# Performance work log

Hardware: AMD Instinct MI355X
Metric: run time of the kernel (lower is better)

The kernel has to match this reference:

```python
import jax, jax.numpy as jnp
import numpy as np

N, E, D, L = 10000, 160000, 512, 3
NEG_SLOPE = 0.2
LN_EPS = 1e-5


def setup_inputs() -> dict:
    key = jax.random.key(0)
    ks = jax.random.split(key, 16)
    def rn(k, shape, scale=0.02):
        return jax.random.normal(k, shape, dtype=jnp.float32) * scale
    return {
        "x": jax.random.normal(ks[0], (N, D), dtype=jnp.float32),
        "edge_attr": jax.random.normal(ks[1], (E, 2), dtype=jnp.float32),
        "emb_inv_W": rn(ks[2], (D, D)), "emb_inv_b": jnp.zeros((D,), jnp.float32),
        "emb_org_W": rn(ks[3], (D, D)), "emb_org_b": jnp.zeros((D,), jnp.float32),
        "gat_Wl": rn(ks[4], (L, D, D)), "gat_bl": jnp.zeros((L, D), jnp.float32),
        "gat_Wr": rn(ks[5], (L, D, D)), "gat_br": jnp.zeros((L, D), jnp.float32),
        "gat_We": rn(ks[6], (L, 2, D)),
        "gat_att": rn(ks[7], (L, D), 0.1),
        "gat_bias": jnp.zeros((L, D), jnp.float32),
        "ln_g": jnp.ones((L, D), jnp.float32), "ln_b": jnp.zeros((L, D), jnp.float32),
        "lin0_W": rn(ks[8], (2 * D, D)), "lin0_b": jnp.zeros((D,), jnp.float32),
        "lin1_W": rn(ks[9], (2 * D, D)), "lin1_b": jnp.zeros((D,), jnp.float32),
        "edge_index": jax.random.randint(ks[10], (2, E), 0, N, dtype=jnp.int32),
        "n_inv": 4000,
        "n_unknown": 3000,
    }


def _layernorm(x, g, b):
    m = jnp.mean(x, axis=-1, keepdims=True)
    v = jnp.mean((x - m) ** 2, axis=-1, keepdims=True)
    return (x - m) * jax.lax.rsqrt(v + LN_EPS) * g + b


def _gatv2(x, src, dst, edge_attr, Wl, bl, Wr, br, We, att, bias):
    # single-head GATv2: e_ij = att . leaky_relu(Wl x_j + Wr x_i + We e_ij)
    xl = x @ Wl + bl                                  # [N,D] source transform
    xr = x @ Wr + br                                  # [N,D] target transform
    m = xl[src] + xr[dst] + edge_attr @ We            # [E,D]
    s = jax.nn.leaky_relu(m, NEG_SLOPE) @ att         # [E] attention logits
    smax = jax.ops.segment_max(s, dst, num_segments=N)  # per-target max
    a = jnp.exp(s - smax[dst])
    denom = jax.ops.segment_sum(a, dst, num_segments=N)
    alpha = a / jnp.where(denom[dst] > 0, denom[dst], 1.0)  # [E]
    out = jax.ops.segment_sum(alpha[:, None] * xl[src], dst, num_segments=N)
    return out + bias


def _forward(x, edge_attr, emb_inv_W, emb_inv_b, emb_org_W, emb_org_b,
             gat_Wl, gat_bl, gat_Wr, gat_br, gat_We, gat_att, gat_bias,
             ln_g, ln_b, lin0_W, lin0_b, lin1_W, lin1_b,
             edge_index, n_inv, n_unknown):
    src, dst = edge_index[0], edge_index[1]
    x0 = x[:n_inv] @ emb_inv_W + emb_inv_b           # [n_inv, D]
    x1 = x[n_inv:] @ emb_org_W + emb_org_b           # [N-n_inv, D]
    h = jnp.concatenate([x0, x1], axis=0)            # [N, D]
    for k in range(L):
        hc = _gatv2(h, src, dst, edge_attr,
                    gat_Wl[k], gat_bl[k], gat_Wr[k], gat_br[k],
                    gat_We[k], gat_att[k], gat_bias[k])
        h = jax.nn.relu(_layernorm(hc + h, ln_g[k], ln_b[k]))
    y0 = jnp.concatenate([x0, h[:n_inv]], axis=-1) @ lin0_W + lin0_b          # [n_inv, D]
    y1 = jnp.concatenate([x1[-n_unknown:], h[-n_unknown:]], axis=-1) @ lin1_W + lin1_b  # [n_unknown, D]
    return y0 @ y1.T                                  # [n_inv, n_unknown]


def reference(x, edge_attr, emb_inv_W, emb_inv_b, emb_org_W, emb_org_b,
              gat_Wl, gat_bl, gat_Wr, gat_br, gat_We, gat_att, gat_bias,
              ln_g, ln_b, lin0_W, lin0_b, lin1_W, lin1_b,
              edge_index, n_inv, n_unknown):
    return _forward(x, edge_attr, emb_inv_W, emb_inv_b, emb_org_W, emb_org_b,
                    gat_Wl, gat_bl, gat_Wr, gat_br, gat_We, gat_att, gat_bias,
                    ln_g, ln_b, lin0_W, lin0_b, lin1_W, lin1_b,
                    edge_index, n_inv, n_unknown)
```

## Files before the change

kernel.cpp:

```cpp
#include <hip/hip_runtime.h>
#include <cstddef>
#include <cstdint>

namespace {

using u16 = unsigned short;
typedef __attribute__((ext_vector_type(8))) unsigned short u16x8;
typedef __attribute__((ext_vector_type(8))) short bf16x8;
typedef __attribute__((ext_vector_type(4))) float f32x4;

constexpr int kN    = 10000;
constexpr int kE    = 160000;
constexpr int kD    = 512;
constexpr int kNinv = 4000;
constexpr int kNunk = 3000;
constexpr int kND   = kN * kD;
constexpr float kNegSlope = 0.2f;
constexpr float kLnEps    = 1e-5f;

__device__ __forceinline__ float bf2f(u16 u) {
  return __uint_as_float((unsigned)u << 16);
}
__device__ __forceinline__ u16 f2bf(float f) {
  unsigned u = __float_as_uint(f);
  return (u16)((u + 0x7FFFu + ((u >> 16) & 1u)) >> 16);
}

__device__ __forceinline__ void gload_lds16(const void* g, void* l) {
  __builtin_amdgcn_global_load_lds(
      (const __attribute__((address_space(1))) void*)(unsigned long long)(uintptr_t)g,
      (__attribute__((address_space(3))) void*)(unsigned)(uintptr_t)l,
      16, 0, 0);
}

template <bool WRITE_F32, bool WRITE_BF16>
__global__ __launch_bounds__(256) void gemm_bf16(
    const u16* __restrict__ A1, const u16* __restrict__ A2,
    const u16* __restrict__ BT, const float* __restrict__ bias,
    float* __restrict__ Cf, u16* __restrict__ Cb, u16* __restrict__ Cb2,
    int nsplit, int M, int N, int K, int ldc) {
  __shared__ u16 As[128 * 64];
  __shared__ u16 Bs[128 * 64];
  const int tid  = threadIdx.x;
  const int lane = tid & 63;
  const int wid  = tid >> 6;
  const int bm = blockIdx.x * 128;
  const int bn = blockIdx.y * 128;
  const int wr = (wid >> 1) * 64;
  const int wc = (wid & 1) * 64;

  f32x4 acc[4][4];
#pragma unroll
  for (int m = 0; m < 4; ++m)
#pragma unroll
    for (int n = 0; n < 4; ++n) acc[m][n] = (f32x4){0.f, 0.f, 0.f, 0.f};

  const int srow = lane >> 3;
  const int slot = lane & 7;
  const size_t astride = (A2 != nullptr) ? 512 : (size_t)K;

  for (int k0 = 0; k0 < K; k0 += 64) {
    const u16* Ap = A1;
    int kof = k0;
    if (A2 != nullptr && k0 >= 512) { Ap = A2; kof = k0 - 512; }
#pragma unroll
    for (int t = 0; t < 4; ++t) {
      const int inst = wid * 4 + t;
      const int row  = inst * 8 + srow;
      const int scol = ((slot ^ (row & 7)) << 4);
      const int ar   = min(bm + row, M - 1);
      gload_lds16((const char*)Ap + ((size_t)ar * astride + kof) * 2 + scol,
                  (char*)As + inst * 1024);
    }
#pragma unroll
    for (int t = 0; t < 4; ++t) {
      const int inst = wid * 4 + t;
      const int row  = inst * 8 + srow;
      const int scol = ((slot ^ (row & 7)) << 4);
      const int bc   = min(bn + row, N - 1);
      gload_lds16((const char*)BT + ((size_t)bc * K + k0) * 2 + scol,
                  (char*)Bs + inst * 1024);
    }
    asm volatile("s_waitcnt vmcnt(0)" ::: "memory");
    __syncthreads();

#pragma unroll
    for (int kk = 0; kk < 2; ++kk) {
      bf16x8 af[4], bfr[4];
#pragma unroll
      for (int m = 0; m < 4; ++m) {
        const int r = wr + m * 16 + (lane & 15);
        const int s = kk * 4 + (lane >> 4);
        af[m] = *(const bf16x8*)((const char*)As + r * 128 + ((s ^ (r & 7)) << 4));
      }
#pragma unroll
      for (int n = 0; n < 4; ++n) {
        const int c = wc + n * 16 + (lane & 15);
        const int s = kk * 4 + (lane >> 4);
        bfr[n] = *(const bf16x8*)((const char*)Bs + c * 128 + ((s ^ (c & 7)) << 4));
      }
#pragma unroll
      for (int m = 0; m < 4; ++m)
#pragma unroll
        for (int n = 0; n < 4; ++n)
          acc[m][n] = __builtin_amdgcn_mfma_f32_16x16x32_bf16(af[m], bfr[n],
                                                              acc[m][n], 0, 0, 0);
    }
    __syncthreads();
  }

#pragma unroll
  for (int m = 0; m < 4; ++m) {
    const int row0 = bm + wr + m * 16 + ((lane >> 4) << 2);
#pragma unroll
    for (int n = 0; n < 4; ++n) {
      const int col = bn + wc + n * 16 + (lane & 15);
      if (col < N) {
        const float bv = (bias != nullptr) ? bias[col] : 0.f;
#pragma unroll
        for (int j = 0; j < 4; ++j) {
          const int r = row0 + j;
          if (r < M) {
            const float v = acc[m][n][j] + bv;
            if (WRITE_F32) Cf[(size_t)r * ldc + col] = v;
            if (WRITE_BF16) {
              u16* dstp = Cb;
              int c = col;
              if (Cb2 != nullptr && col >= nsplit) { dstp = Cb2; c = col - nsplit; }
              dstp[(size_t)r * ldc + c] = f2bf(v);
            }
          }
        }
      }
    }
  }
}

__global__ __launch_bounds__(256) void gat_fused_kernel(
    const u16* __restrict__ xl, const u16* __restrict__ xr,
    const float* __restrict__ ea, const int* __restrict__ src,
    const int* __restrict__ offs, const int* __restrict__ sorted,
    const float* __restrict__ We, const float* __restrict__ att,
    const float* __restrict__ bias, const float* __restrict__ lng,
    const float* __restrict__ lnb, float* __restrict__ hF,
    u16* __restrict__ hb) {
  const int tid = threadIdx.x, wid = tid >> 6, lane = tid & 63;
  const int n = blockIdx.x * 4 + wid;
  if (n >= kN) return;
  const int d8 = lane * 8;

  float r8[8], w0[8], w1[8], a8[8];
  {
    const u16x8 rv = *(const u16x8*)(xr + (size_t)n * kD + d8);
#pragma unroll
    for (int i = 0; i < 8; ++i) {
      r8[i] = bf2f(rv[i]);
      w0[i] = We[d8 + i];
      w1[i] = We[kD + d8 + i];
      a8[i] = att[d8 + i];
    }
  }

  float acc[8];
#pragma unroll
  for (int j = 0; j < 8; ++j) acc[j] = 0.f;
  float m_run = -INFINITY, l_run = 0.f;

  const int beg = offs[n], end = offs[n + 1];
  for (int base = beg; base < end; base += 64) {
    const int cnt = min(64, end - base);
    const int e  = sorted[base + ((lane < cnt) ? lane : 0)];
    const int sv = src[e];
    const float2 e2 = *(const float2*)(ea + (size_t)e * 2);

    u16x8 row = *(const u16x8*)(xl + (size_t)__shfl(sv, 0) * kD + d8);
    for (int i = 0; i < cnt; ++i) {
      u16x8 nrow = row;
      if (i + 1 < cnt) {
        nrow = *(const u16x8*)(xl + (size_t)__shfl(sv, i + 1) * kD + d8);
      }
      const float ex = __shfl(e2.x, i), ey = __shfl(e2.y, i);
      float s = 0.f;
#pragma unroll
      for (int j = 0; j < 8; ++j) {
        const float m = bf2f(row[j]) + r8[j] + ex * w0[j] + ey * w1[j];
        s += a8[j] * (m >= 0.f ? m : kNegSlope * m);
      }
#pragma unroll
      for (int off = 32; off > 0; off >>= 1) s += __shfl_xor(s, off);
      const float nm = fmaxf(m_run, s);
      const float sc = __expf(m_run - nm);
      const float w  = __expf(s - nm);
      l_run = l_run * sc + w;
#pragma unroll
      for (int j = 0; j < 8; ++j) acc[j] = acc[j] * sc + w * bf2f(row[j]);
      m_run = nm;
      row = nrow;
    }
  }

  const float inv = 1.f / (l_run > 0.f ? l_run : 1.f);

  float xv[8];
  float sum = 0.f, sq = 0.f;
  {
    const float4 h0 = *(const float4*)(hF + (size_t)n * kD + d8);
    const float4 h1 = *(const float4*)(hF + (size_t)n * kD + d8 + 4);
    const float hv[8] = {h0.x, h0.y, h0.z, h0.w, h1.x, h1.y, h1.z, h1.w};
#pragma unroll
    for (int j = 0; j < 8; ++j) {
      xv[j] = hv[j] + acc[j] * inv + bias[d8 + j];
      sum += xv[j];
      sq  += xv[j] * xv[j];
    }
  }
#pragma unroll
  for (int off = 32; off > 0; off >>= 1) {
    sum += __shfl_xor(sum, off);
    sq  += __shfl_xor(sq, off);
  }
  const float mean = sum * (1.f / kD);
  const float var  = sq * (1.f / kD) - mean * mean;
  const float rs = rsqrtf(var + kLnEps);
  float y[8];
  u16x8 pk;
#pragma unroll
  for (int j = 0; j < 8; ++j) {
    y[j] = fmaxf((xv[j] - mean) * rs * lng[d8 + j] + lnb[d8 + j], 0.f);
    pk[j] = f2bf(y[j]);
  }
  float4 o0, o1;
  o0.x = y[0]; o0.y = y[1]; o0.z = y[2]; o0.w = y[3];
  o1.x = y[4]; o1.y = y[5]; o1.z = y[6]; o1.w = y[7];
  *(float4*)(hF + (size_t)n * kD + d8)     = o0;
  *(float4*)(hF + (size_t)n * kD + d8 + 4) = o1;
  *(u16x8*)(hb + (size_t)n * kD + d8) = pk;
}

struct TxJobs {
  const float* src[10];
  u16* dst[10];
  int K[10];
};

__global__ __launch_bounds__(256) void transpose_all_kernel(TxJobs jobs) {
  const int z = blockIdx.z;
  const int K = jobs.K[z];
  const int k0 = blockIdx.x * 32;
  if (k0 >= K) return;
  const int n0 = blockIdx.y * 32;
  const float* W = jobs.src[z];
  u16* WT = jobs.dst[z];
  __shared__ float t[32][33];
  const int lx = threadIdx.x & 31, ly = threadIdx.x >> 5;
#pragma unroll
  for (int r = 0; r < 32; r += 8)
    t[ly + r][lx] = W[(size_t)(k0 + ly + r) * 512 + n0 + lx];
  __syncthreads();
#pragma unroll
  for (int r = 0; r < 32; r += 8)
    WT[(size_t)(n0 + ly + r) * K + k0 + lx] = f2bf(t[lx][ly + r]);
}

__global__ void convert_bf16_kernel(const float* __restrict__ in,
                                    u16* __restrict__ out, int n4) {
  const int i = blockIdx.x * 256 + threadIdx.x;
  if (i >= n4) return;
  const float4 v = reinterpret_cast<const float4*>(in)[i];
  u16 o[4] = {f2bf(v.x), f2bf(v.y), f2bf(v.z), f2bf(v.w)};
  *reinterpret_cast<ulonglong1*>(out + (size_t)i * 4) =
      *reinterpret_cast<ulonglong1*>(o);
}

__global__ void catbias_kernel(const float* __restrict__ bl,
                               const float* __restrict__ br,
                               float* __restrict__ catB) {
  const int i = blockIdx.x * 256 + threadIdx.x;
  if (i >= 3 * 1024) return;
  const int k = i >> 10, j = i & 1023;
  catB[i] = (j < 512) ? bl[k * 512 + j] : br[k * 512 + j - 512];
}

__global__ void fill_i32(int* p, int v, int n) {
  const int i = blockIdx.x * 256 + threadIdx.x;
  if (i < n) p[i] = v;
}
__global__ void copy_i32(const int* a, int* b, int n) {
  const int i = blockIdx.x * 256 + threadIdx.x;
  if (i < n) b[i] = a[i];
}
__global__ void count_kernel(const int* __restrict__ dst, int* __restrict__ counts) {
  const int e = blockIdx.x * 256 + threadIdx.x;
  if (e < kE) atomicAdd(&counts[dst[e]], 1);
}
__global__ __launch_bounds__(1024) void scan_kernel(const int* __restrict__ counts,
                                                    int* __restrict__ offs, int n) {
  __shared__ int buf[1024];
  __shared__ int carry;
  const int tid = threadIdx.x;
  if (tid == 0) carry = 0;
  __syncthreads();
  for (int base = 0; base < n; base += 1024) {
    const int v = (base + tid < n) ? counts[base + tid] : 0;
    buf[tid] = v;
    __syncthreads();
    for (int off = 1; off < 1024; off <<= 1) {
      const int t = (tid >= off) ? buf[tid - off] : 0;
      __syncthreads();
      buf[tid] += t;
      __syncthreads();
    }
    if (base + tid < n) offs[base + tid] = carry + buf[tid] - v;
    __syncthreads();
    if (tid == 0) carry += buf[1023];
    __syncthreads();
  }
  if (tid == 0) offs[n] = carry;
}
__global__ void scatter_kernel(const int* __restrict__ dst, int* __restrict__ pos,
                               int* __restrict__ sorted) {
  const int e = blockIdx.x * 256 + threadIdx.x;
  if (e >= kE) return;
  const int p = atomicAdd(&pos[dst[e]], 1);
  sorted[p] = e;
}

}

extern "C" void kernel_launch(void* const* d_in, const int* in_sizes, int n_in,
                              void* d_out, int out_size, void* d_ws, size_t ws_size,
                              hipStream_t stream) {
  const float* x         = (const float*)d_in[0];
  const float* edge_attr = (const float*)d_in[1];
  const float* emb_inv_W = (const float*)d_in[2];
  const float* emb_inv_b = (const float*)d_in[3];
  const float* emb_org_W = (const float*)d_in[4];
  const float* emb_org_b = (const float*)d_in[5];
  const float* gat_Wl    = (const float*)d_in[6];
  const float* gat_bl    = (const float*)d_in[7];
  const float* gat_Wr    = (const float*)d_in[8];
  const float* gat_br    = (const float*)d_in[9];
  const float* gat_We    = (const float*)d_in[10];
  const float* gat_att   = (const float*)d_in[11];
  const float* gat_bias  = (const float*)d_in[12];
  const float* ln_g      = (const float*)d_in[13];
  const float* ln_b      = (const float*)d_in[14];
  const float* lin0_W    = (const float*)d_in[15];
  const float* lin0_b    = (const float*)d_in[16];
  const float* lin1_W    = (const float*)d_in[17];
  const float* lin1_b    = (const float*)d_in[18];
  const int*   edge_idx  = (const int*)d_in[19];
  const int* src = edge_idx;
  const int* dst = edge_idx + kE;
  float* out = (float*)d_out;

  float* hF   = (float*)d_ws;
  float* catB = hF + kND;
  u16* xb   = (u16*)(catB + 3072);
  u16* hb0  = xb + kND;
  u16* hb   = hb0 + kND;
  u16* xlB  = hb + kND;
  u16* xrB  = xlB + kND;
  u16* y0b  = xrB + kND;
  u16* y1b  = y0b + kNinv * kD;
  u16* embInvT = y1b + kNunk * kD;
  u16* embOrgT = embInvT + 262144;
  u16* WlrT    = embOrgT + 262144;
  u16* lin0T   = WlrT + 3 * 524288;
  u16* lin1T   = lin0T + 524288;
  int* counts  = (int*)(lin1T + 524288);
  int* offs    = counts + kN;
  int* pos     = offs + kN + 1;
  int* sorted  = pos + kN;

  const dim3 blk(256);
  auto cdiv = [](int a, int b) { return (a + b - 1) / b; };

  {
    TxJobs j;
    j.src[0] = emb_inv_W;  j.dst[0] = embInvT;  j.K[0] = 512;
    j.src[1] = emb_org_W;  j.dst[1] = embOrgT;  j.K[1] = 512;
    for (int k = 0; k < 3; ++k) {
      j.src[2 + k] = gat_Wl + (size_t)k * kD * kD;
      j.dst[2 + k] = WlrT + (size_t)k * 524288;
      j.K[2 + k] = 512;
      j.src[5 + k] = gat_Wr + (size_t)k * kD * kD;
      j.dst[5 + k] = WlrT + (size_t)k * 524288 + 262144;
      j.K[5 + k] = 512;
    }
    j.src[8] = lin0_W; j.dst[8] = lin0T; j.K[8] = 1024;
    j.src[9] = lin1_W; j.dst[9] = lin1T; j.K[9] = 1024;
    transpose_all_kernel<<<dim3(32, 16, 10), blk, 0, stream>>>(j);
  }
  convert_bf16_kernel<<<dim3(cdiv(kND / 4, 256)), blk, 0, stream>>>(x, xb, kND / 4);
  catbias_kernel<<<dim3(12), blk, 0, stream>>>(gat_bl, gat_br, catB);

  gemm_bf16<true, true><<<dim3(cdiv(kNinv, 128), 4), blk, 0, stream>>>(
      xb, nullptr, embInvT, emb_inv_b, hF, hb0, nullptr, 0, kNinv, kD, kD, kD);
  gemm_bf16<true, true><<<dim3(cdiv(kN - kNinv, 128), 4), blk, 0, stream>>>(
      xb + (size_t)kNinv * kD, nullptr, embOrgT, emb_org_b,
      hF + (size_t)kNinv * kD, hb0 + (size_t)kNinv * kD, nullptr, 0,
      kN - kNinv, kD, kD, kD);

  fill_i32<<<dim3(cdiv(kN, 256)), blk, 0, stream>>>(counts, 0, kN);
  count_kernel<<<dim3(cdiv(kE, 256)), blk, 0, stream>>>(dst, counts);
  scan_kernel<<<dim3(1), dim3(1024), 0, stream>>>(counts, offs, kN);
  copy_i32<<<dim3(cdiv(kN, 256)), blk, 0, stream>>>(offs, pos, kN);
  scatter_kernel<<<dim3(cdiv(kE, 256)), blk, 0, stream>>>(dst, pos, sorted);

  for (int k = 0; k < 3; ++k) {
    const u16* hIn = (k == 0) ? hb0 : hb;
    gemm_bf16<false, true><<<dim3(cdiv(kN, 128), 8), blk, 0, stream>>>(
        hIn, nullptr, WlrT + (size_t)k * 524288, catB + k * 1024,
        nullptr, xlB, xrB, 512, kN, 1024, kD, kD);
    gat_fused_kernel<<<dim3(cdiv(kN, 4)), blk, 0, stream>>>(
        xlB, xrB, edge_attr, src, offs, sorted,
        gat_We + (size_t)k * 2 * kD, gat_att + (size_t)k * kD,
        gat_bias + (size_t)k * kD, ln_g + (size_t)k * kD,
        ln_b + (size_t)k * kD, hF, hb);
  }

  gemm_bf16<false, true><<<dim3(cdiv(kNinv, 128), 4), blk, 0, stream>>>(
      hb0, hb, lin0T, lin0_b, nullptr, y0b, nullptr, 0, kNinv, kD, 2 * kD, kD);
  const size_t off = (size_t)(kN - kNunk) * kD;
  gemm_bf16<false, true><<<dim3(cdiv(kNunk, 128), 4), blk, 0, stream>>>(
      hb0 + off, hb + off, lin1T, lin1_b, nullptr, y1b, nullptr, 0,
      kNunk, kD, 2 * kD, kD);

  gemm_bf16<true, false><<<dim3(cdiv(kNinv, 128), cdiv(kNunk, 128)), blk, 0, stream>>>(
      y0b, nullptr, y1b, nullptr, out, nullptr, nullptr, 0,
      kNinv, kNunk, kD, kNunk);
}
```

Measured before the change: 439.8 us.

## Batch eight gathered edges per step and pre-permute edge source and attributes

The scatter kernel now writes source indices and edge attributes directly in destination-sorted order, which removes the sorted→edge indirection from the GAT kernel. The GAT kernel gathers up to eight neighbour rows at once and reduces their logits together, so more loads are in flight per wave. It also drops the online-softmax running max, which assumes the logits are small enough that exp does not overflow. Leaky-ReLU becomes 0.6m+0.4|m|, and blocks shrink to two waves each.

```diff
diff --git a/kernel.cpp b/kernel.cpp
--- a/kernel.cpp
+++ b/kernel.cpp
@@ -15,8 +15,7 @@
 constexpr int kNinv = 4000;
 constexpr int kNunk = 3000;
 constexpr int kND   = kN * kD;
-constexpr float kNegSlope = 0.2f;
-constexpr float kLnEps    = 1e-5f;
+constexpr float kLnEps = 1e-5f;
 
 __device__ __forceinline__ float bf2f(u16 u) {
   return __uint_as_float((unsigned)u << 16);
@@ -136,20 +135,19 @@
   }
 }
 
-__global__ __launch_bounds__(256) void gat_fused_kernel(
+__global__ __launch_bounds__(128) void gat_fused_kernel(
     const u16* __restrict__ xl, const u16* __restrict__ xr,
-    const float* __restrict__ ea, const int* __restrict__ src,
-    const int* __restrict__ offs, const int* __restrict__ sorted,
-    const float* __restrict__ We, const float* __restrict__ att,
-    const float* __restrict__ bias, const float* __restrict__ lng,
-    const float* __restrict__ lnb, float* __restrict__ hF,
-    u16* __restrict__ hb) {
-  const int tid = threadIdx.x, wid = tid >> 6, lane = tid & 63;
-  const int n = blockIdx.x * 4 + wid;
+    const int* __restrict__ esrcS, const float2* __restrict__ eaS,
+    const int* __restrict__ offs, const float* __restrict__ We,
+    const float* __restrict__ att, const float* __restrict__ bias,
+    const float* __restrict__ lng, const float* __restrict__ lnb,
+    float* __restrict__ hF, u16* __restrict__ hb) {
+  const int wid = threadIdx.x >> 6, lane = threadIdx.x & 63;
+  const int n = blockIdx.x * 2 + wid;
   if (n >= kN) return;
   const int d8 = lane * 8;
 
-  float r8[8], w0[8], w1[8], a8[8];
+  float r8[8], w0[8], w1[8], a06[8], a04[8];
   {
     const u16x8 rv = *(const u16x8*)(xr + (size_t)n * kD + d8);
 #pragma unroll
@@ -157,45 +155,65 @@
       r8[i] = bf2f(rv[i]);
       w0[i] = We[d8 + i];
       w1[i] = We[kD + d8 + i];
-      a8[i] = att[d8 + i];
+      const float a = att[d8 + i];
+      a06[i] = 0.6f * a;
+      a04[i] = 0.4f * a;
     }
   }
 
   float acc[8];
 #pragma unroll
   for (int j = 0; j < 8; ++j) acc[j] = 0.f;
-  float m_run = -INFINITY, l_run = 0.f;
+  float l_run = 0.f;
 
   const int beg = offs[n], end = offs[n + 1];
   for (int base = beg; base < end; base += 64) {
     const int cnt = min(64, end - base);
-    const int e  = sorted[base + ((lane < cnt) ? lane : 0)];
-    const int sv = src[e];
-    const float2 e2 = *(const float2*)(ea + (size_t)e * 2);
-
-    u16x8 row = *(const u16x8*)(xl + (size_t)__shfl(sv, 0) * kD + d8);
-    for (int i = 0; i < cnt; ++i) {
-      u16x8 nrow = row;
-      if (i + 1 < cnt) {
-        nrow = *(const u16x8*)(xl + (size_t)__shfl(sv, i + 1) * kD + d8);
-      }
-      const float ex = __shfl(e2.x, i), ey = __shfl(e2.y, i);
-      float s = 0.f;
+    const int idx = base + ((lane < cnt) ? lane : 0);
+    const int sv = esrcS[idx];
+    const float2 e2 = eaS[idx];
+
+    for (int i = 0; i < cnt; i += 8) {
+      const int k = cnt - i;
+      u16x8 rows[8];
+#pragma unroll
+      for (int t = 0; t < 8; ++t)
+        if (t < k)
+          rows[t] = *(const u16x8*)(xl + (size_t)__shfl(sv, i + t) * kD + d8);
+      float s[8];
+#pragma unroll
+      for (int t = 0; t < 8; ++t) {
+        s[t] = 0.f;
+        if (t < k) {
+          const float ex = __shfl(e2.x, i + t), ey = __shfl(e2.y, i + t);
+#pragma unroll
+          for (int j = 0; j < 8; ++j) {
+            const float m = bf2f(rows[t][j]) + r8[j] + ex * w0[j] + ey * w1[j];
+            s[t] += a06[j] * m + a04[j] * fabsf(m);
+          }
+        }
+      }
+#pragma unroll
+      for (int off = 32; off > 0; off >>= 1)
+#pragma unroll
+        for (int t = 0; t < 8; ++t)
+          if (t < k) s[t] += __shfl_xor(s[t], off);
+      float q[8];
+      float ws = 0.f;
+#pragma unroll
+      for (int t = 0; t < 8; ++t) {
+        q[t] = (t < k) ? __expf(s[t]) : 0.f;
+        ws += q[t];
+      }
+      l_run += ws;
 #pragma unroll
       for (int j = 0; j < 8; ++j) {
-        const float m = bf2f(row[j]) + r8[j] + ex * w0[j] + ey * w1[j];
-        s += a8[j] * (m >= 0.f ? m : kNegSlope * m);
-      }
-#pragma unroll
-      for (int off = 32; off > 0; off >>= 1) s += __shfl_xor(s, off);
-      const float nm = fmaxf(m_run, s);
-      const float sc = __expf(m_run - nm);
-      const float w  = __expf(s - nm);
-      l_run = l_run * sc + w;
-#pragma unroll
-      for (int j = 0; j < 8; ++j) acc[j] = acc[j] * sc + w * bf2f(row[j]);
-      m_run = nm;
-      row = nrow;
+        float v = acc[j];
+#pragma unroll
+        for (int t = 0; t < 8; ++t)
+          if (t < k) v += q[t] * bf2f(rows[t][j]);
+        acc[j] = v;
+      }
     }
   }
 
@@ -317,12 +335,17 @@
   }
   if (tid == 0) offs[n] = carry;
 }
-__global__ void scatter_kernel(const int* __restrict__ dst, int* __restrict__ pos,
-                               int* __restrict__ sorted) {
+__global__ void scatter_kernel(const int* __restrict__ dst,
+                               const int* __restrict__ src,
+                               const float* __restrict__ ea,
+                               int* __restrict__ pos,
+                               int* __restrict__ esrcS,
+                               float2* __restrict__ eaS) {
   const int e = blockIdx.x * 256 + threadIdx.x;
   if (e >= kE) return;
   const int p = atomicAdd(&pos[dst[e]], 1);
-  sorted[p] = e;
+  esrcS[p] = src[e];
+  eaS[p] = *(const float2*)(ea + (size_t)e * 2);
 }
 
 }
@@ -371,7 +394,8 @@
   int* counts  = (int*)(lin1T + 524288);
   int* offs    = counts + kN;
   int* pos     = offs + kN + 1;
-  int* sorted  = pos + kN;
+  int* esrcS   = pos + kN;
+  float2* eaS  = (float2*)(esrcS + kE);
 
   const dim3 blk(256);
   auto cdiv = [](int a, int b) { return (a + b - 1) / b; };
@@ -406,15 +430,16 @@
   count_kernel<<<dim3(cdiv(kE, 256)), blk, 0, stream>>>(dst, counts);
   scan_kernel<<<dim3(1), dim3(1024), 0, stream>>>(counts, offs, kN);
   copy_i32<<<dim3(cdiv(kN, 256)), blk, 0, stream>>>(offs, pos, kN);
-  scatter_kernel<<<dim3(cdiv(kE, 256)), blk, 0, stream>>>(dst, pos, sorted);
+  scatter_kernel<<<dim3(cdiv(kE, 256)), blk, 0, stream>>>(dst, src, edge_attr, pos,
+                                                          esrcS, eaS);
 
   for (int k = 0; k < 3; ++k) {
     const u16* hIn = (k == 0) ? hb0 : hb;
     gemm_bf16<false, true><<<dim3(cdiv(kN, 128), 8), blk, 0, stream>>>(
         hIn, nullptr, WlrT + (size_t)k * 524288, catB + k * 1024,
         nullptr, xlB, xrB, 512, kN, 1024, kD, kD);
-    gat_fused_kernel<<<dim3(cdiv(kN, 4)), blk, 0, stream>>>(
-        xlB, xrB, edge_attr, src, offs, sorted,
+    gat_fused_kernel<<<dim3(cdiv(kN, 2)), dim3(128), 0, stream>>>(
+        xlB, xrB, esrcS, eaS, offs,
         gat_We + (size_t)k * 2 * kD, gat_att + (size_t)k * kD,
         gat_bias + (size_t)k * kD, ln_g + (size_t)k * kD,
         ln_b + (size_t)k * kD, hF, hb);
```

After: 554.4 us. 1.26x slower.
